# Optimization experiments

Measured on AMD Instinct MI355X. Metric: run time of the kernel, lower is better.

## Reference

```python
import jax, jax.numpy as jnp
import numpy as np

EPS = 1e-5
NEG_SLOPE = 0.01


def setup_inputs() -> dict:
    key = jax.random.key(0)
    ks = jax.random.split(key, 5)
    B, T, I, H = 16, 16384, 64, 128
    s = 1.0 / np.sqrt(H)
    return {
        "x": jax.random.normal(ks[0], (B, T, I), dtype=jnp.float32),
        "W_ih": jax.random.normal(ks[1], (4 * H, I), dtype=jnp.float32) * s,
        "W_hh": jax.random.normal(ks[2], (4 * H, H), dtype=jnp.float32) * s,
        "b_ih": jax.random.normal(ks[3], (4 * H,), dtype=jnp.float32) * s,
        "b_hh": jax.random.normal(ks[4], (4 * H,), dtype=jnp.float32) * s,
        "gamma": jnp.ones((H,), dtype=jnp.float32),
        "beta": jnp.zeros((H,), dtype=jnp.float32),
    }


def _lstm(x, W_ih, W_hh, b_ih, b_hh):
    B, T, _ = x.shape
    H = W_hh.shape[1]
    # Precompute input contributions for all timesteps: [B, T, 4H]
    gx = jnp.einsum('bti,gi->btg', x, W_ih) + b_ih + b_hh

    def step(carry, g_t):
        h, c = carry
        g = g_t + h @ W_hh.T  # [B, 4H]
        i, f, gg, o = jnp.split(g, 4, axis=-1)  # PyTorch gate order i,f,g,o
        i = jax.nn.sigmoid(i)
        f = jax.nn.sigmoid(f)
        gg = jnp.tanh(gg)
        o = jax.nn.sigmoid(o)
        c = f * c + i * gg
        h = o * jnp.tanh(c)
        return (h, c), h

    h0 = jnp.zeros((B, H), dtype=x.dtype)
    (hn, cn), out = jax.lax.scan(step, (h0, h0), jnp.swapaxes(gx, 0, 1))
    return jnp.swapaxes(out, 0, 1), hn, cn  # out: [B, T, H]


def reference(x, W_ih, W_hh, b_ih, b_hh, gamma, beta):
    B, T, _ = x.shape
    H = W_hh.shape[1]
    out, hn, cn = _lstm(x, W_ih, W_hh, b_ih, b_hh)
    # BatchNorm1d (training mode) over flattened [B*T, H]
    flat = out.reshape(-1, H)
    mean = flat.mean(axis=0)
    var = flat.var(axis=0)  # biased variance, as PyTorch uses for normalization
    norm = (flat - mean) * jax.lax.rsqrt(var + EPS) * gamma + beta
    y = jax.nn.leaky_relu(norm.reshape(B, T, H), NEG_SLOPE)
    return (y, (hn[None], cn[None]))  # hn/cn: [num_layers=1, B, H]
```

## Files before the change

kernel.cpp:

```cpp
#include <hip/hip_runtime.h>
#include <hip/hip_bf16.h>
#include <cstdint>

#define TB 16
#define TT 16384
#define TI 64
#define TH 128
#define TG 512

typedef _Float16 f16x8 __attribute__((ext_vector_type(8)));
typedef float    f32x4 __attribute__((ext_vector_type(4)));

typedef const float __attribute__((address_space(1)))* gcfp;
typedef float __attribute__((address_space(1)))*       gfp;

__device__ __forceinline__ float sigf(float z) {
    return 1.0f / (1.0f + __expf(-z));
}
__device__ __forceinline__ float tanhf_fast(float z) {
    return 2.0f / (1.0f + __expf(-2.0f * z)) - 1.0f;
}
__device__ __forceinline__ float4 ld4(const float* p) {
    return *reinterpret_cast<const float4*>(p);
}
__device__ __forceinline__ void fma4(float4& acc, const float4 w, const float4 h) {
    acc.x = fmaf(w.x, h.x, acc.x);
    acc.y = fmaf(w.y, h.y, acc.y);
    acc.z = fmaf(w.z, h.z, acc.z);
    acc.w = fmaf(w.w, h.w, acc.w);
}
__device__ __forceinline__ float hsum4(const float4 a) {
    return (a.x + a.y) + (a.z + a.w);
}
__device__ __forceinline__ void pin_agpr(f16x8& v) {
    asm volatile("" : "+a"(v));
}

__global__ __launch_bounds__(256, 2) void gx_precompute(
    const float* __restrict__ x, const float* __restrict__ W_ih,
    const float* __restrict__ b_ih, const float* __restrict__ b_hh,
    float* __restrict__ gx)
{
    const int tid  = threadIdx.x;
    const int j    = tid & (TH - 1);
    const int pair = tid >> 7;
    const int row_a = pair * 2 * TH + j;
    const int row_b = row_a + TH;

    float4 ua[TI / 4], ub[TI / 4];
#pragma unroll
    for (int k4 = 0; k4 < TI / 4; ++k4) {
        ua[k4] = ld4(W_ih + (size_t)row_a * TI + k4 * 4);
        ub[k4] = ld4(W_ih + (size_t)row_b * TI + k4 * 4);
    }
    const float bias_a = b_ih[row_a] + b_hh[row_a];
    const float bias_b = b_ih[row_b] + b_hh[row_b];

    __shared__ __align__(16) float xs[2][TI];
    const int ROWS = 128;
    const size_t r0 = (size_t)blockIdx.x * ROWS;

    if (tid < TI / 4)
        *reinterpret_cast<float4*>(&xs[0][tid * 4]) = ld4(x + r0 * TI + tid * 4);
    __syncthreads();
    float4 xreg = make_float4(0.f, 0.f, 0.f, 0.f);
    if (tid < TI / 4) xreg = ld4(x + (r0 + 1) * TI + tid * 4);

#pragma unroll 1
    for (int rr = 0; rr < ROWS; ++rr) {
        const float* xrow = xs[rr & 1];
        float4 aa = make_float4(0.f, 0.f, 0.f, 0.f);
        float4 ab = make_float4(0.f, 0.f, 0.f, 0.f);
#pragma unroll
        for (int k4 = 0; k4 < TI / 4; ++k4) {
            const float4 x4 = *reinterpret_cast<const float4*>(&xrow[k4 * 4]);
            fma4(aa, ua[k4], x4);
            fma4(ab, ub[k4], x4);
        }
        if (tid < TI / 4) {
            if (rr + 1 < ROWS)
                *reinterpret_cast<float4*>(&xs[(rr + 1) & 1][tid * 4]) = xreg;
            if (rr + 2 < ROWS) xreg = ld4(x + (r0 + rr + 2) * TI + tid * 4);
        }
        float* grow = gx + (r0 + rr) * (size_t)TG;
        grow[row_a] = hsum4(aa) + bias_a;
        grow[row_b] = hsum4(ab) + bias_b;

        asm volatile("s_waitcnt lgkmcnt(0)" ::: "memory");
        __builtin_amdgcn_s_barrier();
    }
}

__global__
__attribute__((amdgpu_flat_work_group_size(320, 320), amdgpu_waves_per_eu(1, 2)))
void lstm_scan_mfma5(
    const float* __restrict__ W_hh, const float* __restrict__ gx,
    float* __restrict__ y, float* __restrict__ hn, float* __restrict__ cn)
{
    const int b    = blockIdx.x;
    const int tid  = threadIdx.x;
    const int w    = tid >> 6;
    const int lane = tid & 63;
    const int c    = lane & 15;
    const int oct  = lane >> 4;
    const int uu   = oct & 1;
    const int ch   = 32 * (w & 3) + 16 * uu + c;

    __shared__ __align__(16) _Float16 h_lds[2][TH];
    __shared__ __align__(16) float    gx_lds[2][TG];

    float c_state = 0.0f;
    float h_keep  = 0.0f;

    f16x8 bf[4][2][4];
    float4 va, vb;
    const float4* g4 = reinterpret_cast<const float4*>(gx + (size_t)b * TT * TG);

    if (w < 4) {
#pragma unroll
        for (int s = 0; s < 4; ++s) {
#pragma unroll
            for (int u = 0; u < 2; ++u) {
#pragma unroll
                for (int kt = 0; kt < 4; ++kt) {
                    const float* wr = W_hh +
                        (size_t)(s * TH + 32 * w + 16 * u + c) * TH + kt * 32 + oct * 8;
                    const float4 lo = ld4(wr);
                    const float4 hi = ld4(wr + 4);
                    bf[s][u][kt] = f16x8{(_Float16)lo.x, (_Float16)lo.y,
                                         (_Float16)lo.z, (_Float16)lo.w,
                                         (_Float16)hi.x, (_Float16)hi.y,
                                         (_Float16)hi.z, (_Float16)hi.w};
                }
            }
        }
#pragma unroll
        for (int s = 0; s < 4; ++s)
#pragma unroll
            for (int u = 0; u < 2; ++u)
#pragma unroll
                for (int kt = 0; kt < 4; ++kt) pin_agpr(bf[s][u][kt]);

        if (tid < TH) h_lds[0][tid] = (_Float16)0.f;
    } else {
        va = g4[lane];
        vb = g4[lane + 64];
        *reinterpret_cast<float4*>(&gx_lds[0][lane * 4])       = va;
        *reinterpret_cast<float4*>(&gx_lds[0][256 + lane * 4]) = vb;
        va = g4[128 + lane];
        vb = g4[128 + lane + 64];
        g4 += 256;
    }

    asm volatile("s_waitcnt lgkmcnt(0)" ::: "memory");
    __builtin_amdgcn_s_barrier();

    const f32x4 kz = {0.f, 0.f, 0.f, 0.f};

    if (w < 4) {
        gfp yp = (gfp)(y + (size_t)b * TT * TH + ch);

#define CSTEP(S)                                                               \
    {                                                                          \
        f16x8 a0 = *(const f16x8*)&h_lds[S][0 * 32 + oct * 8];                 \
        f16x8 a1 = *(const f16x8*)&h_lds[S][1 * 32 + oct * 8];                 \
        f16x8 a2 = *(const f16x8*)&h_lds[S][2 * 32 + oct * 8];                 \
        f16x8 a3 = *(const f16x8*)&h_lds[S][3 * 32 + oct * 8];                 \
        const float g0 = gx_lds[S][0 * TH + ch];                               \
        const float g1 = gx_lds[S][1 * TH + ch];                               \
        const float g2 = gx_lds[S][2 * TH + ch];                               \
        const float g3 = gx_lds[S][3 * TH + ch];                               \
        float pv[4][2];                                                        \
        _Pragma("unroll")                                                      \
        for (int s = 0; s < 4; ++s) {                                          \
            _Pragma("unroll")                                                  \
            for (int u = 0; u < 2; ++u) {                                      \
                f32x4 qa = __builtin_amdgcn_mfma_f32_16x16x32_f16(             \
                    a0, bf[s][u][0], kz, 0, 0, 0);                             \
                qa = __builtin_amdgcn_mfma_f32_16x16x32_f16(                   \
                    a1, bf[s][u][1], qa, 0, 0, 0);                             \
                f32x4 qb = __builtin_amdgcn_mfma_f32_16x16x32_f16(             \
                    a2, bf[s][u][2], kz, 0, 0, 0);                             \
                qb = __builtin_amdgcn_mfma_f32_16x16x32_f16(                   \
                    a3, bf[s][u][3], qb, 0, 0, 0);                             \
                pv[s][u] = qa[0] + qb[0];                                      \
            }                                                                  \
        }                                                                      \
        const float p0 = (uu ? pv[0][1] : pv[0][0]) + g0;                      \
        const float p1 = (uu ? pv[1][1] : pv[1][0]) + g1;                      \
        const float p2 = (uu ? pv[2][1] : pv[2][0]) + g2;                      \
        const float p3 = (uu ? pv[3][1] : pv[3][0]) + g3;                      \
        const float gi = sigf(p0);                                             \
        const float gf = sigf(p1);                                             \
        const float gg = tanhf_fast(p2);                                       \
        const float go = sigf(p3);                                             \
        c_state = fmaf(gf, c_state, gi * gg);                                  \
        h_keep  = go * tanhf_fast(c_state);                                    \
        if (lane < 32) {                                                       \
            h_lds[S ^ 1][ch] = (_Float16)h_keep;                               \
            *yp = h_keep;                                                      \
        }                                                                      \
        yp += TH;                                                              \
        asm volatile("s_waitcnt lgkmcnt(0)" ::: "memory");                     \
        __builtin_amdgcn_s_barrier();                                          \
    }

#pragma unroll 1
        for (int t = 0; t < TT; t += 2) {
            CSTEP(0)
            CSTEP(1)
        }
#undef CSTEP

        if (lane < 32) {
            ((gfp)(hn))[(size_t)b * TH + ch] = h_keep;
            ((gfp)(cn))[(size_t)b * TH + ch] = c_state;
        }
    } else {
#define PSTEP(S)                                                               \
    {                                                                          \
                    \
        *reinterpret_cast<float4*>(&gx_lds[S ^ 1][lane * 4])       = va;       \
        *reinterpret_cast<float4*>(&gx_lds[S ^ 1][256 + lane * 4]) = vb;       \
        va = g4[lane];                                                         \
        vb = g4[lane + 64];                                                    \
        g4 += 128;                                                             \
        asm volatile("s_waitcnt lgkmcnt(0)" ::: "memory");                     \
        __builtin_amdgcn_s_barrier();                                          \
    }

#pragma unroll 1
        for (int t = 0; t < TT; t += 2) {
            PSTEP(0)
            PSTEP(1)
        }
#undef PSTEP
    }
}

__global__ __launch_bounds__(512, 2) void lstm_scan_fused(
    const float* __restrict__ x, const float* __restrict__ W_ih,
    const float* __restrict__ W_hh, const float* __restrict__ b_ih,
    const float* __restrict__ b_hh,
    float* __restrict__ y, float* __restrict__ hn, float* __restrict__ cn)
{
    const int b    = blockIdx.x;
    const int tid  = threadIdx.x;
    const int j    = tid & (TH - 1);
    const int gate = tid >> 7;

    __shared__ __align__(16) float h_lds[TH];
    __shared__ __align__(16) float g_lds[TG];
    __shared__ __align__(16) float xs[2][TI];

    float4 w[TH / 4];
#pragma unroll
    for (int k4 = 0; k4 < TH / 4; ++k4)
        w[k4] = ld4(W_hh + (size_t)tid * TH + k4 * 4);
    float4 u[TI / 4];
#pragma unroll
    for (int k4 = 0; k4 < TI / 4; ++k4)
        u[k4] = ld4(W_ih + (size_t)tid * TI + k4 * 4);
    const float bias = b_ih[tid] + b_hh[tid];

    if (tid < TH) h_lds[tid] = 0.0f;
    float c_state = 0.0f;
    float h_keep  = 0.0f;

    float4 xreg = make_float4(0.f, 0.f, 0.f, 0.f);
    const float* xp = x + ((size_t)b * TT + 2) * TI;
    float* yp = y + (size_t)b * TT * TH;

    if (tid < TI / 4)
        *reinterpret_cast<float4*>(&xs[0][tid * 4]) =
            ld4(x + ((size_t)b * TT + 0) * TI + tid * 4);
    __syncthreads();
    if (tid < TI / 4)
        xreg = ld4(x + ((size_t)b * TT + 1) * TI + tid * 4);

#pragma unroll 1
    for (int t = 0; t < TT; ++t) {
        float4 acc = make_float4(0.f, 0.f, 0.f, 0.f);
#pragma unroll
        for (int k4 = 0; k4 < TH / 4; ++k4) {
            const float4 h4 = *reinterpret_cast<const float4*>(&h_lds[k4 * 4]);
            fma4(acc, w[k4], h4);
        }
        float p = hsum4(acc);
        {
            float4 fx = make_float4(0.f, 0.f, 0.f, 0.f);
            const float* xrow = xs[t & 1];
#pragma unroll
            for (int k4 = 0; k4 < TI / 4; ++k4) {
                const float4 x4 = *reinterpret_cast<const float4*>(&xrow[k4 * 4]);
                fma4(fx, u[k4], x4);
            }
            p += hsum4(fx) + bias;
        }

        const float act = (gate == 2) ? tanhf_fast(p) : sigf(p);
        g_lds[tid] = act;

        asm volatile("s_waitcnt lgkmcnt(0)" ::: "memory");
        __builtin_amdgcn_s_barrier();

        if (tid < TH) {
            const float gi = g_lds[j];
            const float gf = g_lds[TH + j];
            const float gg = g_lds[2 * TH + j];
            const float go = g_lds[3 * TH + j];
            c_state = fmaf(gf, c_state, gi * gg);
            h_keep  = go * tanhf_fast(c_state);
            h_lds[j] = h_keep;
            yp[(size_t)t * TH + j] = h_keep;
        }

        if (tid < TI / 4) {
            if (t + 1 < TT)
                *reinterpret_cast<float4*>(&xs[(t + 1) & 1][tid * 4]) = xreg;
            if (t + 2 < TT) xreg = ld4(xp + tid * 4);
        }
        xp += TI;

        asm volatile("s_waitcnt lgkmcnt(0)" ::: "memory");
        __builtin_amdgcn_s_barrier();
    }

    if (tid < TH) {
        hn[(size_t)b * TH + j] = h_keep;
        cn[(size_t)b * TH + j] = c_state;
    }
}

__global__ void bn_zero(float* ws) { ws[threadIdx.x] = 0.0f; }

__global__ __launch_bounds__(256) void bn_stats(const float* __restrict__ y,
                                                float* __restrict__ ws)
{
    const int tid  = threadIdx.x;
    const int col4 = tid & 31;
    const int rg   = tid >> 5;
    const int NROW = TB * TT;
    float4 s = make_float4(0.f, 0.f, 0.f, 0.f);
    float4 q = make_float4(0.f, 0.f, 0.f, 0.f);
    for (int row = blockIdx.x * 8 + rg; row < NROW; row += gridDim.x * 8) {
        const float4 v = ld4(y + (size_t)row * TH + col4 * 4);
        s.x += v.x; s.y += v.y; s.z += v.z; s.w += v.w;
        q.x = fmaf(v.x, v.x, q.x); q.y = fmaf(v.y, v.y, q.y);
        q.z = fmaf(v.z, v.z, q.z); q.w = fmaf(v.w, v.w, q.w);
    }
    __shared__ float4 ls[256], lq[256];
    ls[tid] = s; lq[tid] = q;
    __syncthreads();
    if (tid < 32) {
        float4 S = ls[tid], Q = lq[tid];
        for (int g2 = 1; g2 < 8; ++g2) {
            const float4 a = ls[g2 * 32 + tid], b2 = lq[g2 * 32 + tid];
            S.x += a.x; S.y += a.y; S.z += a.z; S.w += a.w;
            Q.x += b2.x; Q.y += b2.y; Q.z += b2.z; Q.w += b2.w;
        }
        atomicAdd(&ws[tid * 4 + 0], S.x); atomicAdd(&ws[tid * 4 + 1], S.y);
        atomicAdd(&ws[tid * 4 + 2], S.z); atomicAdd(&ws[tid * 4 + 3], S.w);
        atomicAdd(&ws[TH + tid * 4 + 0], Q.x); atomicAdd(&ws[TH + tid * 4 + 1], Q.y);
        atomicAdd(&ws[TH + tid * 4 + 2], Q.z); atomicAdd(&ws[TH + tid * 4 + 3], Q.w);
    }
}

__global__ __launch_bounds__(256) void bn_apply(float* __restrict__ y,
                                                const float* __restrict__ ws,
                                                const float* __restrict__ gamma,
                                                const float* __restrict__ beta)
{
    const int tid  = threadIdx.x;
    const int col4 = tid & 31;
    const int rg   = tid >> 5;
    const int NROW = TB * TT;
    const float invN = 1.0f / (float)(TB * TT);

    const float4 sm = ld4(ws + col4 * 4);
    const float4 sq = ld4(ws + TH + col4 * 4);
    const float4 gm = ld4(gamma + col4 * 4);
    const float4 bt = ld4(beta + col4 * 4);
    float4 mean, scale, shift;
    mean.x = sm.x * invN; mean.y = sm.y * invN;
    mean.z = sm.z * invN; mean.w = sm.w * invN;
    scale.x = rsqrtf(fmaf(-mean.x, mean.x, sq.x * invN) + 1e-5f) * gm.x;
    scale.y = rsqrtf(fmaf(-mean.y, mean.y, sq.y * invN) + 1e-5f) * gm.y;
    scale.z = rsqrtf(fmaf(-mean.z, mean.z, sq.z * invN) + 1e-5f) * gm.z;
    scale.w = rsqrtf(fmaf(-mean.w, mean.w, sq.w * invN) + 1e-5f) * gm.w;
    shift.x = bt.x - mean.x * scale.x; shift.y = bt.y - mean.y * scale.y;
    shift.z = bt.z - mean.z * scale.z; shift.w = bt.w - mean.w * scale.w;

    for (int row = blockIdx.x * 8 + rg; row < NROW; row += gridDim.x * 8) {
        float* p = y + (size_t)row * TH + col4 * 4;
        float4 v = *reinterpret_cast<const float4*>(p);
        v.x = fmaf(v.x, scale.x, shift.x); v.y = fmaf(v.y, scale.y, shift.y);
        v.z = fmaf(v.z, scale.z, shift.z); v.w = fmaf(v.w, scale.w, shift.w);
        v.x = fmaxf(v.x, 0.01f * v.x); v.y = fmaxf(v.y, 0.01f * v.y);
        v.z = fmaxf(v.z, 0.01f * v.z); v.w = fmaxf(v.w, 0.01f * v.w);
        *reinterpret_cast<float4*>(p) = v;
    }
}

extern "C" void kernel_launch(void* const* d_in, const int* in_sizes, int n_in,
                              void* d_out, int out_size, void* d_ws, size_t ws_size,
                              hipStream_t stream)
{
    const float* x     = (const float*)d_in[0];
    const float* W_ih  = (const float*)d_in[1];
    const float* W_hh  = (const float*)d_in[2];
    const float* b_ih  = (const float*)d_in[3];
    const float* b_hh  = (const float*)d_in[4];
    const float* gamma = (const float*)d_in[5];
    const float* beta  = (const float*)d_in[6];

    float* y  = (float*)d_out;
    float* hn = y + (size_t)TB * TT * TH;
    float* cn = hn + TB * TH;

    float* ws_stats = (float*)d_ws;
    const size_t GX_BYTES = (size_t)TB * TT * TG * sizeof(float);
    const bool use_ws = ws_size >= GX_BYTES + 4096 + 4 * TG * sizeof(float);

    bn_zero<<<1, 256, 0, stream>>>(ws_stats);

    if (use_ws) {
        float* gxbuf = (float*)((char*)d_ws + 4096);
        gx_precompute<<<2048, 256, 0, stream>>>(x, W_ih, b_ih, b_hh, gxbuf);
        lstm_scan_mfma5<<<TB, 320, 0, stream>>>(W_hh, gxbuf, y, hn, cn);
    } else {
        lstm_scan_fused<<<TB, 512, 0, stream>>>(x, W_ih, W_hh, b_ih, b_hh,
                                                y, hn, cn);
    }

    bn_stats<<<512, 256, 0, stream>>>(y, ws_stats);
    bn_apply<<<2048, 256, 0, stream>>>(y, ws_stats, gamma, beta);
}
```

Before: 9.048 ms.

## Pack two batch sequences per workgroup in LSTM scan kernel

```diff
diff --git a/kernel.cpp b/kernel.cpp
--- a/kernel.cpp
+++ b/kernel.cpp
@@ -92,22 +92,24 @@
 }
 
 __global__
-__attribute__((amdgpu_flat_work_group_size(320, 320), amdgpu_waves_per_eu(1, 2)))
-void lstm_scan_mfma5(
+__attribute__((amdgpu_flat_work_group_size(640, 640), amdgpu_waves_per_eu(2, 3)))
+void lstm_scan_mfma6(
     const float* __restrict__ W_hh, const float* __restrict__ gx,
     float* __restrict__ y, float* __restrict__ hn, float* __restrict__ cn)
 {
-    const int b    = blockIdx.x;
     const int tid  = threadIdx.x;
     const int w    = tid >> 6;
+    const int grp  = (w >= 5);
+    const int wg   = w - 5 * grp;
     const int lane = tid & 63;
     const int c    = lane & 15;
     const int oct  = lane >> 4;
     const int uu   = oct & 1;
-    const int ch   = 32 * (w & 3) + 16 * uu + c;
-
-    __shared__ __align__(16) _Float16 h_lds[2][TH];
-    __shared__ __align__(16) float    gx_lds[2][TG];
+    const int ch   = 32 * (wg & 3) + 16 * uu + c;
+    const int b    = 2 * blockIdx.x + grp;
+
+    __shared__ __align__(16) _Float16 h_lds[2][2][TH];
+    __shared__ __align__(16) float    gx_lds[2][2][TG];
 
     float c_state = 0.0f;
     float h_keep  = 0.0f;
@@ -116,7 +118,7 @@
     float4 va, vb;
     const float4* g4 = reinterpret_cast<const float4*>(gx + (size_t)b * TT * TG);
 
-    if (w < 4) {
+    if (wg < 4) {
 #pragma unroll
         for (int s = 0; s < 4; ++s) {
 #pragma unroll
@@ -124,7 +126,7 @@
 #pragma unroll
                 for (int kt = 0; kt < 4; ++kt) {
                     const float* wr = W_hh +
-                        (size_t)(s * TH + 32 * w + 16 * u + c) * TH + kt * 32 + oct * 8;
+                        (size_t)(s * TH + 32 * wg + 16 * u + c) * TH + kt * 32 + oct * 8;
                     const float4 lo = ld4(wr);
                     const float4 hi = ld4(wr + 4);
                     bf[s][u][kt] = f16x8{(_Float16)lo.x, (_Float16)lo.y,
@@ -141,12 +143,15 @@
 #pragma unroll
                 for (int kt = 0; kt < 4; ++kt) pin_agpr(bf[s][u][kt]);
 
-        if (tid < TH) h_lds[0][tid] = (_Float16)0.f;
+        if (wg == 0 && lane < 64) {
+            h_lds[grp][0][lane]      = (_Float16)0.f;
+            h_lds[grp][0][lane + 64] = (_Float16)0.f;
+        }
     } else {
         va = g4[lane];
         vb = g4[lane + 64];
-        *reinterpret_cast<float4*>(&gx_lds[0][lane * 4])       = va;
-        *reinterpret_cast<float4*>(&gx_lds[0][256 + lane * 4]) = vb;
+        *reinterpret_cast<float4*>(&gx_lds[grp][0][lane * 4])       = va;
+        *reinterpret_cast<float4*>(&gx_lds[grp][0][256 + lane * 4]) = vb;
         va = g4[128 + lane];
         vb = g4[128 + lane + 64];
         g4 += 256;
@@ -157,19 +162,19 @@
 
     const f32x4 kz = {0.f, 0.f, 0.f, 0.f};
 
-    if (w < 4) {
+    if (wg < 4) {
         gfp yp = (gfp)(y + (size_t)b * TT * TH + ch);
 
 #define CSTEP(S)                                                               \
     {                                                                          \
-        f16x8 a0 = *(const f16x8*)&h_lds[S][0 * 32 + oct * 8];                 \
-        f16x8 a1 = *(const f16x8*)&h_lds[S][1 * 32 + oct * 8];                 \
-        f16x8 a2 = *(const f16x8*)&h_lds[S][2 * 32 + oct * 8];                 \
-        f16x8 a3 = *(const f16x8*)&h_lds[S][3 * 32 + oct * 8];                 \
-        const float g0 = gx_lds[S][0 * TH + ch];                               \
-        const float g1 = gx_lds[S][1 * TH + ch];                               \
-        const float g2 = gx_lds[S][2 * TH + ch];                               \
-        const float g3 = gx_lds[S][3 * TH + ch];                               \
+        f16x8 a0 = *(const f16x8*)&h_lds[grp][S][0 * 32 + oct * 8];            \
+        f16x8 a1 = *(const f16x8*)&h_lds[grp][S][1 * 32 + oct * 8];            \
+        f16x8 a2 = *(const f16x8*)&h_lds[grp][S][2 * 32 + oct * 8];            \
+        f16x8 a3 = *(const f16x8*)&h_lds[grp][S][3 * 32 + oct * 8];            \
+        const float g0 = gx_lds[grp][S][0 * TH + ch];                          \
+        const float g1 = gx_lds[grp][S][1 * TH + ch];                          \
+        const float g2 = gx_lds[grp][S][2 * TH + ch];                          \
+        const float g3 = gx_lds[grp][S][3 * TH + ch];                          \
         float pv[4][2];                                                        \
         _Pragma("unroll")                                                      \
         for (int s = 0; s < 4; ++s) {                                          \
@@ -197,7 +202,7 @@
         c_state = fmaf(gf, c_state, gi * gg);                                  \
         h_keep  = go * tanhf_fast(c_state);                                    \
         if (lane < 32) {                                                       \
-            h_lds[S ^ 1][ch] = (_Float16)h_keep;                               \
+            h_lds[grp][S ^ 1][ch] = (_Float16)h_keep;                          \
             *yp = h_keep;                                                      \
         }                                                                      \
         yp += TH;                                                              \
@@ -219,9 +224,8 @@
     } else {
 #define PSTEP(S)                                                               \
     {                                                                          \
-                    \
-        *reinterpret_cast<float4*>(&gx_lds[S ^ 1][lane * 4])       = va;       \
-        *reinterpret_cast<float4*>(&gx_lds[S ^ 1][256 + lane * 4]) = vb;       \
+        *reinterpret_cast<float4*>(&gx_lds[grp][S ^ 1][lane * 4])       = va;  \
+        *reinterpret_cast<float4*>(&gx_lds[grp][S ^ 1][256 + lane * 4]) = vb;  \
         va = g4[lane];                                                         \
         vb = g4[lane + 64];                                                    \
         g4 += 128;                                                             \
@@ -427,7 +431,7 @@
     if (use_ws) {
         float* gxbuf = (float*)((char*)d_ws + 4096);
         gx_precompute<<<2048, 256, 0, stream>>>(x, W_ih, b_ih, b_hh, gxbuf);
-        lstm_scan_mfma5<<<TB, 320, 0, stream>>>(W_hh, gxbuf, y, hn, cn);
+        lstm_scan_mfma6<<<TB / 2, 640, 0, stream>>>(W_hh, gxbuf, y, hn, cn);
     } else {
         lstm_scan_fused<<<TB, 512, 0, stream>>>(x, W_ih, W_hh, b_ih, b_hh,
                                                 y, hn, cn);
```

Measured after the change: 22.62 ms. 150% more time.
